# Performance work log

Hardware: AMD Instinct MI355X
Metric: run time of the kernel (lower is better)

Reference implementation:

```python
import jax, jax.numpy as jnp
import numpy as np
from jax import lax

BETA = 5.0
THRESHOLD = 20.0

def softplus5(x):
    # torch nn.Softplus(beta=5, threshold=20)
    return jnp.where(BETA * x > THRESHOLD, x, jax.nn.softplus(BETA * x) / BETA)

def setup_inputs() -> dict:
    key = jax.random.key(0)
    k1, k2, k3, k4, k5 = jax.random.split(key, 5)
    B, T, I, H = 128, 256, 1024, 1024
    stdv = 1.0 / np.sqrt(H)
    x = jax.random.normal(k1, (B, T, I), dtype=jnp.float32)
    hidden = jnp.zeros((2, B, H), dtype=jnp.float32)
    Wi = jax.random.uniform(k2, (H, I), dtype=jnp.float32, minval=-stdv, maxval=stdv)
    bi = jax.random.uniform(k3, (H,), dtype=jnp.float32, minval=-stdv, maxval=stdv)
    Wh = jax.random.uniform(k4, (H, H), dtype=jnp.float32, minval=-stdv, maxval=stdv)
    bh = jax.random.uniform(k5, (H,), dtype=jnp.float32, minval=-stdv, maxval=stdv)
    return {"x": x, "hidden": hidden, "Wi": Wi, "bi": bi, "Wh": Wh, "bh": bh}

def reference(x, hidden, Wi, bi, Wh, bh):
    # x: [B, T, I] (batch_first) -> time-major [T, B, I]
    xt = jnp.swapaxes(x, 0, 1)
    T = xt.shape[0]
    # precompute i2h for all steps (one big GEMM)
    pre = jnp.einsum('tbi,hi->tbh', xt, Wi) + bi  # [T, B, H]

    def step(h, p):
        h_next = softplus5(p + h @ Wh.T + bh)
        return h_next, h_next

    _, fwd = lax.scan(step, hidden[0], pre)          # fwd[t]: hidden after step t
    _, bwd = lax.scan(step, hidden[1], pre[::-1])    # bwd[j]: backward hidden at time i = T-1-j
    # bi_outputs appended for i = T-1 ... 0: position t holds cat(outputs[(T-1-t)-16], bwd[t])
    idx = (jnp.arange(T)[::-1] - 16) % T  # Python negative-index wrap of outputs[i-16]
    out = jnp.concatenate([fwd[idx], bwd], axis=-1)  # [T, B, 2H]
    return jnp.swapaxes(out, 0, 1)                   # [B, T, 2H]
```

## Files before the change

### kernel.cpp

```cpp
#include <hip/hip_runtime.h>
#include <stddef.h>

using short8 = __attribute__((ext_vector_type(8))) short;
using f32x4  = __attribute__((ext_vector_type(4))) float;
using f32x16 = __attribute__((ext_vector_type(16))) float;
using u16x4  = __attribute__((ext_vector_type(4))) unsigned short;

__device__ __forceinline__ unsigned short cvt_bf16(float f) {
    unsigned u = __builtin_bit_cast(unsigned, f);
    u += 0x7fffu + ((u >> 16) & 1u);
    return (unsigned short)(u >> 16);
}

__device__ __forceinline__ void gload_lds16(const void* g, void* l) {
    __builtin_amdgcn_global_load_lds(
        (const __attribute__((address_space(1))) unsigned*)g,
        (__attribute__((address_space(3))) unsigned*)l, 16, 0, 0);
}

#define MFMA16(a, b, c) __builtin_amdgcn_mfma_f32_16x16x32_bf16((a), (b), (c), 0, 0, 0)
#define MFMA32(a, b, c) __builtin_amdgcn_mfma_f32_32x32x16_bf16((a), (b), (c), 0, 0, 0)

__global__ __launch_bounds__(256) void convert_w(const float* __restrict__ Wi,
                                                 const float* __restrict__ Wh,
                                                 unsigned short* __restrict__ Wib,
                                                 unsigned short* __restrict__ Whb) {
    const float* src = blockIdx.y ? Wh : Wi;
    unsigned short* dst = blockIdx.y ? Whb : Wib;
    int base = blockIdx.x * 2048 + threadIdx.x * 8;
#pragma unroll
    for (int c = 0; c < 2; ++c) {
        float4 v = *(const float4*)(src + base + c * 4);
        u16x4 o;
        o.x = cvt_bf16(v.x); o.y = cvt_bf16(v.y); o.z = cvt_bf16(v.z); o.w = cvt_bf16(v.w);
        *(u16x4*)(dst + base + c * 4) = o;
    }
}

__global__ __launch_bounds__(256) void init_h(const float* __restrict__ hidden,
                                              unsigned short* __restrict__ h0,
                                              unsigned* __restrict__ flags) {
    int row = blockIdx.x;
    int tid = threadIdx.x;
    float4 v = *(const float4*)(hidden + (size_t)row * 1024 + tid * 4);
    u16x4 o;
    o.x = cvt_bf16(v.x); o.y = cvt_bf16(v.y); o.z = cvt_bf16(v.z); o.w = cvt_bf16(v.w);
    *(u16x4*)(h0 + (size_t)row * 1024 + tid * 4) = o;
    if (blockIdx.x == 0 && tid < 256) flags[tid] = 0;
}

__global__ __launch_bounds__(256) void pre_gemm(const float* __restrict__ x,
                                                const unsigned short* __restrict__ Wib,
                                                const float* __restrict__ bi,
                                                float* __restrict__ pre) {
    __shared__ unsigned short Alds[128 * 64];
    __shared__ unsigned short Blds[128 * 64];
    const int tid  = threadIdx.x;
    const int lane = tid & 63, wid = tid >> 6;
    const int wr = wid >> 1, wc = wid & 1;
    const int t  = blockIdx.y;
    const int n0 = blockIdx.x * 128;

    f32x4 acc[4][4] = {};

    for (int kt = 0; kt < 16; ++kt) {
        const int k0 = kt * 64;
        __syncthreads();
#pragma unroll
        for (int c = 0; c < 8; ++c) {
            int flat = c * 256 + tid;
            int row = flat >> 4;
            int seg = flat & 15;
            float4 v = *(const float4*)(x + (size_t)row * 262144 + (size_t)t * 1024 + k0 + seg * 4);
            u16x4 h;
            h.x = cvt_bf16(v.x); h.y = cvt_bf16(v.y); h.z = cvt_bf16(v.z); h.w = cvt_bf16(v.w);
            *(u16x4*)&Alds[row * 64 + seg * 4] = h;
        }
#pragma unroll
        for (int c = 0; c < 4; ++c) {
            int flat = c * 256 + tid;
            int row = flat >> 3;
            int seg = flat & 7;
            gload_lds16(Wib + (size_t)(n0 + row) * 1024 + k0 + seg * 8, &Blds[flat * 8]);
        }
        __syncthreads();
#pragma unroll
        for (int ks = 0; ks < 2; ++ks) {
            short8 a[4], b[4];
#pragma unroll
            for (int i = 0; i < 4; ++i)
                a[i] = *(const short8*)&Alds[(wr * 64 + i * 16 + (lane & 15)) * 64 + ks * 32 + (lane >> 4) * 8];
#pragma unroll
            for (int j = 0; j < 4; ++j)
                b[j] = *(const short8*)&Blds[(wc * 64 + j * 16 + (lane & 15)) * 64 + ks * 32 + (lane >> 4) * 8];
#pragma unroll
            for (int i = 0; i < 4; ++i)
#pragma unroll
                for (int j = 0; j < 4; ++j)
                    acc[i][j] = MFMA16(a[i], b[j], acc[i][j]);
        }
    }
    const int rbase = wr * 64 + (lane >> 4) * 4;
    const int cbase = n0 + wc * 64 + (lane & 15);
#pragma unroll
    for (int i = 0; i < 4; ++i) {
#pragma unroll
        for (int j = 0; j < 4; ++j) {
            int n = cbase + j * 16;
            float bv = bi[n];
#pragma unroll
            for (int r = 0; r < 4; ++r) {
                int m = rbase + i * 16 + r;
                pre[((size_t)t * 128 + m) * 1024 + n] = acc[i][j][r] + bv;
            }
        }
    }
}

__global__ __launch_bounds__(256, 1) void rnn_scan(const unsigned short* __restrict__ Whb,
                                                   const float* __restrict__ pre,
                                                   const float* __restrict__ bh,
                                                   unsigned short* __restrict__ ha,
                                                   unsigned short* __restrict__ hb,
                                                   float* __restrict__ out,
                                                   unsigned* __restrict__ flags) {
    __shared__ unsigned short Alds[32 * 1024];
    __shared__ float Red[4][1024];

    const int tid  = threadIdx.x;
    const int lane = tid & 63, wid = tid >> 6;
    const int bid  = blockIdx.x;
    const int g    = bid & 7, ni = bid >> 3;
    const int m0   = g * 32, n0 = ni * 32;
    const bool fwd = (g < 4);
    unsigned* gflags = flags + g * 32;

    short8 bfrag[16];
    {
        const unsigned short* bp = Whb + (size_t)(n0 + (lane & 31)) * 1024
                                 + wid * 256 + (lane >> 5) * 8;
#pragma unroll
        for (int ks = 0; ks < 16; ++ks)
            bfrag[ks] = *(const short8*)(bp + ks * 16);
    }

    const int mloc = tid >> 3;
    const int nloc = (tid & 7) * 4;
    const int m    = m0 + mloc;
    const int b    = m & 127;
    const int n    = n0 + nloc;
    const float4 bh4 = *(const float4*)(bh + n);
    float* outp      = out + (size_t)b * 524288 + (fwd ? 0 : 1024) + n;
    const float* prebase = pre + (size_t)b * 1024 + n;

    const char* aswz_base = (const char*)Alds + (lane & 31) * 2048;
    const int   aswz      = (lane & 7) << 4;
    const int   kb0       = wid * 512 + (lane >> 5) * 16;

    for (int s = 0; s < 256; ++s) {
        const unsigned short* hin = (s & 1) ? hb : ha;
        unsigned short* hout      = (s & 1) ? ha : hb;
        const int prow = fwd ? s : 255 - s;
        float4 pv = *(const float4*)(prebase + (size_t)prow * 131072);

        if (s > 0) {
            if (tid < 64) {
                int fuel = 1 << 20;
                unsigned v;
                do {
                    v = __hip_atomic_load(&gflags[lane & 31], __ATOMIC_RELAXED,
                                          __HIP_MEMORY_SCOPE_AGENT);
                } while (!__all((int)(v >= (unsigned)s)) && --fuel);
            }
            __syncthreads();
        }

        {
            const unsigned long long* hsrc =
                (const unsigned long long*)(hin + (size_t)m0 * 1024);
            const int colswz = tid * 8;
            unsigned long long tmp[32];
#pragma unroll
            for (int i = 0; i < 32; ++i)
                tmp[i] = __hip_atomic_load(&hsrc[(size_t)i * 256 + tid],
                                           __ATOMIC_RELAXED, __HIP_MEMORY_SCOPE_AGENT);
#pragma unroll
            for (int i = 0; i < 32; ++i)
                *(unsigned long long*)((char*)Alds + i * 2048
                                       + (colswz ^ ((i & 7) << 4))) = tmp[i];
        }
        __syncthreads();

        f32x16 acc0 = {}, acc1 = {};
#pragma unroll
        for (int ks = 0; ks < 16; ++ks) {
            short8 a = *(const short8*)(aswz_base + ((kb0 + ks * 32) ^ aswz));
            if (ks & 1) acc1 = MFMA32(a, bfrag[ks], acc1);
            else        acc0 = MFMA32(a, bfrag[ks], acc0);
        }
        f32x16 acc = acc0 + acc1;
#pragma unroll
        for (int r = 0; r < 16; ++r) {
            int row = (r & 3) + 8 * (r >> 2) + 4 * (lane >> 5);
            Red[wid][row * 32 + (lane & 31)] = acc[r];
        }
        __syncthreads();

        f32x4 ov;
        {
            const int o = tid * 4;
            float4 q0 = *(const float4*)&Red[0][o];
            float4 q1 = *(const float4*)&Red[1][o];
            float4 q2 = *(const float4*)&Red[2][o];
            float4 q3 = *(const float4*)&Red[3][o];
            float vv[4] = { q0.x + q1.x + q2.x + q3.x + pv.x + bh4.x,
                            q0.y + q1.y + q2.y + q3.y + pv.y + bh4.y,
                            q0.z + q1.z + q2.z + q3.z + pv.z + bh4.z,
                            q0.w + q1.w + q2.w + q3.w + pv.w + bh4.w };
            u16x4 hh;
#pragma unroll
            for (int j = 0; j < 4; ++j) {
                float xv = vv[j];
                float hv = (5.0f * xv > 20.0f) ? xv : 0.2f * log1pf(__expf(5.0f * xv));
                ov[j] = hv;
                hh[j] = cvt_bf16(hv);
            }
            __hip_atomic_store((unsigned long long*)(hout + (size_t)m * 1024 + n),
                               __builtin_bit_cast(unsigned long long, hh),
                               __ATOMIC_RELAXED, __HIP_MEMORY_SCOPE_AGENT);
        }
        asm volatile("s_waitcnt vmcnt(0)" ::: "memory");
        __syncthreads();

        if (s < 255 && tid == 0)
            __hip_atomic_store(&gflags[ni], (unsigned)(s + 1),
                               __ATOMIC_RELAXED, __HIP_MEMORY_SCOPE_AGENT);

        int tout = fwd ? ((239 - s) & 255) : s;
        __builtin_nontemporal_store(ov, (f32x4*)(outp + (size_t)tout * 2048));
    }
}

extern "C" void kernel_launch(void* const* d_in, const int* in_sizes, int n_in,
                              void* d_out, int out_size, void* d_ws, size_t ws_size,
                              hipStream_t stream) {
    const float* x      = (const float*)d_in[0];
    const float* hidden = (const float*)d_in[1];
    const float* Wi     = (const float*)d_in[2];
    const float* bi     = (const float*)d_in[3];
    const float* Wh     = (const float*)d_in[4];
    const float* bh     = (const float*)d_in[5];
    float* out = (float*)d_out;

    char* ws = (char*)d_ws;
    float*          pre = (float*)ws;
    unsigned short* Wib = (unsigned short*)(ws + 134217728);
    unsigned short* Whb = (unsigned short*)(ws + 136314880);
    unsigned short* ha  = (unsigned short*)(ws + 138412032);
    unsigned short* hb  = (unsigned short*)(ws + 138936320);
    unsigned*     flags = (unsigned*)(ws + 139460608);

    convert_w<<<dim3(512, 2), 256, 0, stream>>>(Wi, Wh, Wib, Whb);
    init_h<<<256, 256, 0, stream>>>(hidden, ha, flags);
    pre_gemm<<<dim3(8, 256), 256, 0, stream>>>(x, Wib, bi, pre);
    rnn_scan<<<256, 256, 0, stream>>>(Whb, pre, bh, ha, hb, out, flags);
}
```

Baseline: 1.214 ms.

## Use XCD-local cache-scoped sync when all group blocks share one XCD

At startup each block records its XCD id, read from a hardware register, into a workspace slot. Each 32-block group then checks whether all its members landed on the same XCD. If they did, the per-step flag polling and hidden-state exchange use plain loads and stores with the sc0 bit instead of agent-scope atomics, so traffic can stay in the shared L2 rather than going through device-coherent paths. The output stores also change from nontemporal to regular stores. The risks are relying on block placement, adding a startup handshake, and coherence correctness if the co-location check is wrong.

```diff
diff --git a/kernel.cpp b/kernel.cpp
--- a/kernel.cpp
+++ b/kernel.cpp
@@ -46,7 +46,9 @@
     u16x4 o;
     o.x = cvt_bf16(v.x); o.y = cvt_bf16(v.y); o.z = cvt_bf16(v.z); o.w = cvt_bf16(v.w);
     *(u16x4*)(h0 + (size_t)row * 1024 + tid * 4) = o;
-    if (blockIdx.x == 0 && tid < 256) flags[tid] = 0;
+    if (blockIdx.x == 0) {
+        for (int i = tid; i < 512; i += 256) flags[i] = 0;
+    }
 }
 
 __global__ __launch_bounds__(256) void pre_gemm(const float* __restrict__ x,
@@ -126,6 +128,7 @@
                                                    unsigned* __restrict__ flags) {
     __shared__ unsigned short Alds[32 * 1024];
     __shared__ float Red[4][1024];
+    __shared__ int coloc_sh;
 
     const int tid  = threadIdx.x;
     const int lane = tid & 63, wid = tid >> 6;
@@ -133,7 +136,25 @@
     const int g    = bid & 7, ni = bid >> 3;
     const int m0   = g * 32, n0 = ni * 32;
     const bool fwd = (g < 4);
-    unsigned* gflags = flags + g * 32;
+    unsigned* gflags  = flags + g * 32;
+    unsigned* xcdslot = flags + 256;
+
+    if (tid == 0) {
+        unsigned x = __builtin_amdgcn_s_getreg(6164);
+        __hip_atomic_store(&xcdslot[bid], x + 1u, __ATOMIC_RELAXED, __HIP_MEMORY_SCOPE_AGENT);
+    }
+    if (tid < 64) {
+        unsigned v; int fuel = 1 << 22;
+        do {
+            v = __hip_atomic_load(&xcdslot[g * 32 + (lane & 31)],
+                                  __ATOMIC_RELAXED, __HIP_MEMORY_SCOPE_AGENT);
+        } while (__any((int)(v == 0u)) && --fuel);
+        unsigned v0 = __shfl(v, 0);
+        int c = __all((int)(v == v0));
+        if (tid == 0) coloc_sh = c;
+    }
+    __syncthreads();
+    const int coloc = coloc_sh;
 
     short8 bfrag[16];
     {
@@ -165,12 +186,19 @@
 
         if (s > 0) {
             if (tid < 64) {
-                int fuel = 1 << 20;
+                const unsigned* fp = &gflags[lane & 31];
+                int fuel = 1 << 22;
                 unsigned v;
-                do {
-                    v = __hip_atomic_load(&gflags[lane & 31], __ATOMIC_RELAXED,
-                                          __HIP_MEMORY_SCOPE_AGENT);
-                } while (!__all((int)(v >= (unsigned)s)) && --fuel);
+                if (coloc) {
+                    do {
+                        asm volatile("global_load_dword %0, %1, off sc0\n\ts_waitcnt vmcnt(0)"
+                                     : "=v"(v) : "v"(fp) : "memory");
+                    } while (!__all((int)(v >= (unsigned)s)) && --fuel);
+                } else {
+                    do {
+                        v = __hip_atomic_load(fp, __ATOMIC_RELAXED, __HIP_MEMORY_SCOPE_AGENT);
+                    } while (!__all((int)(v >= (unsigned)s)) && --fuel);
+                }
             }
             __syncthreads();
         }
@@ -178,12 +206,21 @@
         {
             const unsigned long long* hsrc =
                 (const unsigned long long*)(hin + (size_t)m0 * 1024);
+            unsigned long long tmp[32];
+            if (coloc) {
+#pragma unroll
+                for (int i = 0; i < 32; ++i)
+                    asm volatile("global_load_dwordx2 %0, %1, off sc0"
+                                 : "=v"(tmp[i]) : "v"(hsrc + (size_t)i * 256 + tid) : "memory");
+                asm volatile("s_waitcnt vmcnt(0)" ::: "memory");
+                __builtin_amdgcn_sched_barrier(0);
+            } else {
+#pragma unroll
+                for (int i = 0; i < 32; ++i)
+                    tmp[i] = __hip_atomic_load(&hsrc[(size_t)i * 256 + tid],
+                                               __ATOMIC_RELAXED, __HIP_MEMORY_SCOPE_AGENT);
+            }
             const int colswz = tid * 8;
-            unsigned long long tmp[32];
-#pragma unroll
-            for (int i = 0; i < 32; ++i)
-                tmp[i] = __hip_atomic_load(&hsrc[(size_t)i * 256 + tid],
-                                           __ATOMIC_RELAXED, __HIP_MEMORY_SCOPE_AGENT);
 #pragma unroll
             for (int i = 0; i < 32; ++i)
                 *(unsigned long long*)((char*)Alds + i * 2048
@@ -225,19 +262,31 @@
                 ov[j] = hv;
                 hh[j] = cvt_bf16(hv);
             }
-            __hip_atomic_store((unsigned long long*)(hout + (size_t)m * 1024 + n),
-                               __builtin_bit_cast(unsigned long long, hh),
-                               __ATOMIC_RELAXED, __HIP_MEMORY_SCOPE_AGENT);
+            unsigned long long hv64 = __builtin_bit_cast(unsigned long long, hh);
+            unsigned short* hp = hout + (size_t)m * 1024 + n;
+            if (coloc) {
+                asm volatile("global_store_dwordx2 %0, %1, off"
+                             :: "v"(hp), "v"(hv64) : "memory");
+            } else {
+                __hip_atomic_store((unsigned long long*)hp, hv64,
+                                   __ATOMIC_RELAXED, __HIP_MEMORY_SCOPE_AGENT);
+            }
         }
         asm volatile("s_waitcnt vmcnt(0)" ::: "memory");
         __syncthreads();
 
-        if (s < 255 && tid == 0)
-            __hip_atomic_store(&gflags[ni], (unsigned)(s + 1),
-                               __ATOMIC_RELAXED, __HIP_MEMORY_SCOPE_AGENT);
+        if (s < 255 && tid == 0) {
+            if (coloc) {
+                asm volatile("global_store_dword %0, %1, off"
+                             :: "v"(&gflags[ni]), "v"((unsigned)(s + 1)) : "memory");
+            } else {
+                __hip_atomic_store(&gflags[ni], (unsigned)(s + 1),
+                                   __ATOMIC_RELAXED, __HIP_MEMORY_SCOPE_AGENT);
+            }
+        }
 
         int tout = fwd ? ((239 - s) & 255) : s;
-        __builtin_nontemporal_store(ov, (f32x4*)(outp + (size_t)tout * 2048));
+        *(f32x4*)(outp + (size_t)tout * 2048) = ov;
     }
 }
 
```

New measurement: 1.239 ms. +2.1%, slower.

## Restructure RNN scan to full-K per wave, fewer blocks and flags

Applied to the files above, without the earlier changes.

The recurrent scan changes from 256 blocks, each splitting K across four waves and reducing through LDS, to 64 blocks where each wave owns 32 output columns over the full K=1024. Each wave keeps 64 weight fragments in registers. This removes the cross-wave LDS reduction and one barrier per step, and cuts the number of flags each group polls from 32 to 8, which should lower per-step synchronisation latency. The costs are much higher register pressure (64 short8 fragments), 4x more MFMAs in sequence per wave, and fewer CUs sharing the work. Output stores also change from nontemporal to plain stores.

```diff
diff --git a/kernel.cpp b/kernel.cpp
--- a/kernel.cpp
+++ b/kernel.cpp
@@ -46,7 +46,9 @@
     u16x4 o;
     o.x = cvt_bf16(v.x); o.y = cvt_bf16(v.y); o.z = cvt_bf16(v.z); o.w = cvt_bf16(v.w);
     *(u16x4*)(h0 + (size_t)row * 1024 + tid * 4) = o;
-    if (blockIdx.x == 0 && tid < 256) flags[tid] = 0;
+    if (blockIdx.x == 0) {
+        for (int i = tid; i < 512; i += 256) flags[i] = 0;
+    }
 }
 
 __global__ __launch_bounds__(256) void pre_gemm(const float* __restrict__ x,
@@ -125,107 +127,95 @@
                                                    float* __restrict__ out,
                                                    unsigned* __restrict__ flags) {
     __shared__ unsigned short Alds[32 * 1024];
-    __shared__ float Red[4][1024];
 
     const int tid  = threadIdx.x;
     const int lane = tid & 63, wid = tid >> 6;
     const int bid  = blockIdx.x;
-    const int g    = bid & 7, ni = bid >> 3;
-    const int m0   = g * 32, n0 = ni * 32;
+    const int g    = bid & 7, ci = bid >> 3;
+    const int m0   = g * 32;
+    const int nw   = ci * 128 + wid * 32;
     const bool fwd = (g < 4);
-    unsigned* gflags = flags + g * 32;
-
-    short8 bfrag[16];
+    unsigned* gflags = flags + g * 8;
+
+    short8 wfrag[64];
     {
-        const unsigned short* bp = Whb + (size_t)(n0 + (lane & 31)) * 1024
-                                 + wid * 256 + (lane >> 5) * 8;
-#pragma unroll
-        for (int ks = 0; ks < 16; ++ks)
-            bfrag[ks] = *(const short8*)(bp + ks * 16);
-    }
-
-    const int mloc = tid >> 3;
-    const int nloc = (tid & 7) * 4;
-    const int m    = m0 + mloc;
-    const int b    = m & 127;
-    const int n    = n0 + nloc;
-    const float4 bh4 = *(const float4*)(bh + n);
-    float* outp      = out + (size_t)b * 524288 + (fwd ? 0 : 1024) + n;
-    const float* prebase = pre + (size_t)b * 1024 + n;
-
-    const char* aswz_base = (const char*)Alds + (lane & 31) * 2048;
-    const int   aswz      = (lane & 7) << 4;
-    const int   kb0       = wid * 512 + (lane >> 5) * 16;
+        const unsigned short* bp = Whb + (size_t)(nw + (lane & 31)) * 1024 + (lane >> 5) * 8;
+#pragma unroll
+        for (int ks = 0; ks < 64; ++ks)
+            wfrag[ks] = *(const short8*)(bp + ks * 16);
+    }
+
+    const int m   = lane & 31;
+    const int mg  = m0 + m;
+    const int b   = mg & 127;
+    const int nhi = (lane >> 5) * 4;
+    f32x4 bh4[4];
+#pragma unroll
+    for (int q = 0; q < 4; ++q)
+        bh4[q] = *(const f32x4*)(bh + nw + nhi + q * 8);
+    const float* prebase = pre + (size_t)b * 1024 + nw + nhi;
+    float* outbase       = out + (size_t)b * 524288 + (fwd ? 0 : 1024) + nw + nhi;
+
+    const char* arow = (const char*)Alds + m * 2048;
+    const int   swz  = (m & 15) << 4;
 
     for (int s = 0; s < 256; ++s) {
         const unsigned short* hin = (s & 1) ? hb : ha;
         unsigned short* hout      = (s & 1) ? ha : hb;
         const int prow = fwd ? s : 255 - s;
-        float4 pv = *(const float4*)(prebase + (size_t)prow * 131072);
+
+        f32x4 pv[4];
+#pragma unroll
+        for (int q = 0; q < 4; ++q)
+            pv[q] = *(const f32x4*)(prebase + (size_t)prow * 131072 + q * 8);
 
         if (s > 0) {
-            if (tid < 64) {
-                int fuel = 1 << 20;
-                unsigned v;
-                do {
-                    v = __hip_atomic_load(&gflags[lane & 31], __ATOMIC_RELAXED,
-                                          __HIP_MEMORY_SCOPE_AGENT);
-                } while (!__all((int)(v >= (unsigned)s)) && --fuel);
-            }
-            __syncthreads();
+            int fuel = 1 << 22;
+            unsigned v;
+            do {
+                v = __hip_atomic_load(&gflags[lane & 7], __ATOMIC_RELAXED,
+                                      __HIP_MEMORY_SCOPE_AGENT);
+            } while (!__all((int)(v >= (unsigned)s)) && --fuel);
         }
 
         {
             const unsigned long long* hsrc =
                 (const unsigned long long*)(hin + (size_t)m0 * 1024);
-            const int colswz = tid * 8;
             unsigned long long tmp[32];
 #pragma unroll
             for (int i = 0; i < 32; ++i)
                 tmp[i] = __hip_atomic_load(&hsrc[(size_t)i * 256 + tid],
                                            __ATOMIC_RELAXED, __HIP_MEMORY_SCOPE_AGENT);
+            const int colswz = tid * 8;
 #pragma unroll
             for (int i = 0; i < 32; ++i)
                 *(unsigned long long*)((char*)Alds + i * 2048
-                                       + (colswz ^ ((i & 7) << 4))) = tmp[i];
+                                       + (colswz ^ ((i & 15) << 4))) = tmp[i];
         }
         __syncthreads();
 
         f32x16 acc0 = {}, acc1 = {};
-#pragma unroll
-        for (int ks = 0; ks < 16; ++ks) {
-            short8 a = *(const short8*)(aswz_base + ((kb0 + ks * 32) ^ aswz));
-            if (ks & 1) acc1 = MFMA32(a, bfrag[ks], acc1);
-            else        acc0 = MFMA32(a, bfrag[ks], acc0);
+        const int khi = (lane >> 5) * 16;
+#pragma unroll
+        for (int ks = 0; ks < 64; ++ks) {
+            short8 hf = *(const short8*)(arow + ((ks * 32 + khi) ^ swz));
+            if (ks & 1) acc1 = MFMA32(wfrag[ks], hf, acc1);
+            else        acc0 = MFMA32(wfrag[ks], hf, acc0);
         }
         f32x16 acc = acc0 + acc1;
-#pragma unroll
-        for (int r = 0; r < 16; ++r) {
-            int row = (r & 3) + 8 * (r >> 2) + 4 * (lane >> 5);
-            Red[wid][row * 32 + (lane & 31)] = acc[r];
-        }
-        __syncthreads();
-
-        f32x4 ov;
-        {
-            const int o = tid * 4;
-            float4 q0 = *(const float4*)&Red[0][o];
-            float4 q1 = *(const float4*)&Red[1][o];
-            float4 q2 = *(const float4*)&Red[2][o];
-            float4 q3 = *(const float4*)&Red[3][o];
-            float vv[4] = { q0.x + q1.x + q2.x + q3.x + pv.x + bh4.x,
-                            q0.y + q1.y + q2.y + q3.y + pv.y + bh4.y,
-                            q0.z + q1.z + q2.z + q3.z + pv.z + bh4.z,
-                            q0.w + q1.w + q2.w + q3.w + pv.w + bh4.w };
+
+        f32x4 ov[4];
+#pragma unroll
+        for (int q = 0; q < 4; ++q) {
             u16x4 hh;
 #pragma unroll
             for (int j = 0; j < 4; ++j) {
-                float xv = vv[j];
+                float xv = acc[q * 4 + j] + pv[q][j] + bh4[q][j];
                 float hv = (5.0f * xv > 20.0f) ? xv : 0.2f * log1pf(__expf(5.0f * xv));
-                ov[j] = hv;
+                ov[q][j] = hv;
                 hh[j] = cvt_bf16(hv);
             }
-            __hip_atomic_store((unsigned long long*)(hout + (size_t)m * 1024 + n),
+            __hip_atomic_store((unsigned long long*)(hout + (size_t)mg * 1024 + nw + nhi + q * 8),
                                __builtin_bit_cast(unsigned long long, hh),
                                __ATOMIC_RELAXED, __HIP_MEMORY_SCOPE_AGENT);
         }
@@ -233,11 +223,13 @@
         __syncthreads();
 
         if (s < 255 && tid == 0)
-            __hip_atomic_store(&gflags[ni], (unsigned)(s + 1),
+            __hip_atomic_store(&gflags[ci], (unsigned)(s + 1),
                                __ATOMIC_RELAXED, __HIP_MEMORY_SCOPE_AGENT);
 
-        int tout = fwd ? ((239 - s) & 255) : s;
-        __builtin_nontemporal_store(ov, (f32x4*)(outp + (size_t)tout * 2048));
+        const int tout = fwd ? ((239 - s) & 255) : s;
+#pragma unroll
+        for (int q = 0; q < 4; ++q)
+            *(f32x4*)(outbase + (size_t)tout * 2048 + q * 8) = ov[q];
     }
 }
 
@@ -263,5 +255,5 @@
     convert_w<<<dim3(512, 2), 256, 0, stream>>>(Wi, Wh, Wib, Whb);
     init_h<<<256, 256, 0, stream>>>(hidden, ha, flags);
     pre_gemm<<<dim3(8, 256), 256, 0, stream>>>(x, Wib, bi, pre);
-    rnn_scan<<<256, 256, 0, stream>>>(Whb, pre, bh, ha, hb, out, flags);
-}
+    rnn_scan<<<64, 256, 0, stream>>>(Whb, pre, bh, ha, hb, out, flags);
+}
```

Result: slower. 2.695 ms (+122.0%).

## Load recurrent A fragments directly from global and finalize in one wave

Applied to the files above, without the earlier changes.

Drops the LDS staging of the hidden-state tile, so each wave spins on the flags itself and loads its MFMA A-operand fragments straight from global memory with atomic loads. The epilogue (reduction, softplus, h store, flag publish, output store) now runs only in wave 0, which removes two block-wide barriers per step. The trade-off is uncoalesced 8-byte global loads and four separate spinning waves, a single wave doing all the epilogue work, and a larger spin limit. It also looks like a hazard on the Red buffer, since the next step's writes are no longer fenced against wave 0's reads.

```diff
diff --git a/kernel.cpp b/kernel.cpp
--- a/kernel.cpp
+++ b/kernel.cpp
@@ -5,6 +5,8 @@
 using f32x4  = __attribute__((ext_vector_type(4))) float;
 using f32x16 = __attribute__((ext_vector_type(16))) float;
 using u16x4  = __attribute__((ext_vector_type(4))) unsigned short;
+
+struct U128 { unsigned long long a, b; };
 
 __device__ __forceinline__ unsigned short cvt_bf16(float f) {
     unsigned u = __builtin_bit_cast(unsigned, f);
@@ -46,7 +48,9 @@
     u16x4 o;
     o.x = cvt_bf16(v.x); o.y = cvt_bf16(v.y); o.z = cvt_bf16(v.z); o.w = cvt_bf16(v.w);
     *(u16x4*)(h0 + (size_t)row * 1024 + tid * 4) = o;
-    if (blockIdx.x == 0 && tid < 256) flags[tid] = 0;
+    if (blockIdx.x == 0) {
+        for (int i = tid; i < 512; i += 256) flags[i] = 0;
+    }
 }
 
 __global__ __launch_bounds__(256) void pre_gemm(const float* __restrict__ x,
@@ -124,7 +128,6 @@
                                                    unsigned short* __restrict__ hb,
                                                    float* __restrict__ out,
                                                    unsigned* __restrict__ flags) {
-    __shared__ unsigned short Alds[32 * 1024];
     __shared__ float Red[4][1024];
 
     const int tid  = threadIdx.x;
@@ -144,57 +147,55 @@
             bfrag[ks] = *(const short8*)(bp + ks * 16);
     }
 
-    const int mloc = tid >> 3;
-    const int nloc = (tid & 7) * 4;
-    const int m    = m0 + mloc;
-    const int b    = m & 127;
-    const int n    = n0 + nloc;
-    const float4 bh4 = *(const float4*)(bh + n);
-    float* outp      = out + (size_t)b * 524288 + (fwd ? 0 : 1024) + n;
-    const float* prebase = pre + (size_t)b * 1024 + n;
-
-    const char* aswz_base = (const char*)Alds + (lane & 31) * 2048;
-    const int   aswz      = (lane & 7) << 4;
-    const int   kb0       = wid * 512 + (lane >> 5) * 16;
+    const size_t arow_off = (size_t)(lane & 31) * 2048 + wid * 512 + (lane >> 5) * 16;
+
+    const int em  = lane >> 1;
+    const int en  = (lane & 1) * 16;
+    const int emg = m0 + em;
+    const int eb  = emg & 127;
+    f32x4 bh4[4];
+#pragma unroll
+    for (int q = 0; q < 4; ++q)
+        bh4[q] = *(const f32x4*)(bh + n0 + en + q * 4);
+    const float* prebase = pre + (size_t)eb * 1024 + n0 + en;
+    float* outbase       = out + (size_t)eb * 524288 + (fwd ? 0 : 1024) + n0 + en;
 
     for (int s = 0; s < 256; ++s) {
         const unsigned short* hin = (s & 1) ? hb : ha;
         unsigned short* hout      = (s & 1) ? ha : hb;
         const int prow = fwd ? s : 255 - s;
-        float4 pv = *(const float4*)(prebase + (size_t)prow * 131072);
+
+        f32x4 pv[4];
+        if (wid == 0) {
+#pragma unroll
+            for (int q = 0; q < 4; ++q)
+                pv[q] = *(const f32x4*)(prebase + (size_t)prow * 131072 + q * 4);
+        }
 
         if (s > 0) {
-            if (tid < 64) {
-                int fuel = 1 << 20;
-                unsigned v;
-                do {
-                    v = __hip_atomic_load(&gflags[lane & 31], __ATOMIC_RELAXED,
-                                          __HIP_MEMORY_SCOPE_AGENT);
-                } while (!__all((int)(v >= (unsigned)s)) && --fuel);
-            }
-            __syncthreads();
-        }
-
-        {
-            const unsigned long long* hsrc =
-                (const unsigned long long*)(hin + (size_t)m0 * 1024);
-            const int colswz = tid * 8;
-            unsigned long long tmp[32];
-#pragma unroll
-            for (int i = 0; i < 32; ++i)
-                tmp[i] = __hip_atomic_load(&hsrc[(size_t)i * 256 + tid],
-                                           __ATOMIC_RELAXED, __HIP_MEMORY_SCOPE_AGENT);
-#pragma unroll
-            for (int i = 0; i < 32; ++i)
-                *(unsigned long long*)((char*)Alds + i * 2048
-                                       + (colswz ^ ((i & 7) << 4))) = tmp[i];
-        }
-        __syncthreads();
+            int fuel = 1 << 22;
+            unsigned v;
+            do {
+                v = __hip_atomic_load(&gflags[lane & 31], __ATOMIC_RELAXED,
+                                      __HIP_MEMORY_SCOPE_AGENT);
+            } while (!__all((int)(v >= (unsigned)s)) && --fuel);
+        }
+
+        const char* hsrc = (const char*)(hin + (size_t)m0 * 1024) + arow_off;
+        unsigned long long alo[16], ahi[16];
+#pragma unroll
+        for (int i = 0; i < 16; ++i) {
+            alo[i] = __hip_atomic_load((const unsigned long long*)(hsrc + i * 32),
+                                       __ATOMIC_RELAXED, __HIP_MEMORY_SCOPE_AGENT);
+            ahi[i] = __hip_atomic_load((const unsigned long long*)(hsrc + i * 32 + 8),
+                                       __ATOMIC_RELAXED, __HIP_MEMORY_SCOPE_AGENT);
+        }
 
         f32x16 acc0 = {}, acc1 = {};
 #pragma unroll
         for (int ks = 0; ks < 16; ++ks) {
-            short8 a = *(const short8*)(aswz_base + ((kb0 + ks * 32) ^ aswz));
+            U128 t2{alo[ks], ahi[ks]};
+            short8 a = __builtin_bit_cast(short8, t2);
             if (ks & 1) acc1 = MFMA32(a, bfrag[ks], acc1);
             else        acc0 = MFMA32(a, bfrag[ks], acc0);
         }
@@ -206,38 +207,39 @@
         }
         __syncthreads();
 
-        f32x4 ov;
-        {
-            const int o = tid * 4;
-            float4 q0 = *(const float4*)&Red[0][o];
-            float4 q1 = *(const float4*)&Red[1][o];
-            float4 q2 = *(const float4*)&Red[2][o];
-            float4 q3 = *(const float4*)&Red[3][o];
-            float vv[4] = { q0.x + q1.x + q2.x + q3.x + pv.x + bh4.x,
-                            q0.y + q1.y + q2.y + q3.y + pv.y + bh4.y,
-                            q0.z + q1.z + q2.z + q3.z + pv.z + bh4.z,
-                            q0.w + q1.w + q2.w + q3.w + pv.w + bh4.w };
-            u16x4 hh;
-#pragma unroll
-            for (int j = 0; j < 4; ++j) {
-                float xv = vv[j];
-                float hv = (5.0f * xv > 20.0f) ? xv : 0.2f * log1pf(__expf(5.0f * xv));
-                ov[j] = hv;
-                hh[j] = cvt_bf16(hv);
+        if (wid == 0) {
+            f32x4 ov[4];
+#pragma unroll
+            for (int q = 0; q < 4; ++q) {
+                const int o = (em * 32 + en) + q * 4;
+                f32x4 v0 = *(const f32x4*)&Red[0][o];
+                f32x4 v1 = *(const f32x4*)&Red[1][o];
+                f32x4 v2 = *(const f32x4*)&Red[2][o];
+                f32x4 v3 = *(const f32x4*)&Red[3][o];
+                f32x4 vv = v0 + v1 + v2 + v3 + pv[q] + bh4[q];
+                u16x4 hh;
+#pragma unroll
+                for (int j = 0; j < 4; ++j) {
+                    float xv = vv[j];
+                    float hv = (5.0f * xv > 20.0f) ? xv : 0.2f * log1pf(__expf(5.0f * xv));
+                    ov[q][j] = hv;
+                    hh[j] = cvt_bf16(hv);
+                }
+                __hip_atomic_store(
+                    (unsigned long long*)(hout + (size_t)emg * 1024 + n0 + en + q * 4),
+                    __builtin_bit_cast(unsigned long long, hh),
+                    __ATOMIC_RELAXED, __HIP_MEMORY_SCOPE_AGENT);
             }
-            __hip_atomic_store((unsigned long long*)(hout + (size_t)m * 1024 + n),
-                               __builtin_bit_cast(unsigned long long, hh),
-                               __ATOMIC_RELAXED, __HIP_MEMORY_SCOPE_AGENT);
-        }
-        asm volatile("s_waitcnt vmcnt(0)" ::: "memory");
-        __syncthreads();
-
-        if (s < 255 && tid == 0)
-            __hip_atomic_store(&gflags[ni], (unsigned)(s + 1),
-                               __ATOMIC_RELAXED, __HIP_MEMORY_SCOPE_AGENT);
-
-        int tout = fwd ? ((239 - s) & 255) : s;
-        __builtin_nontemporal_store(ov, (f32x4*)(outp + (size_t)tout * 2048));
+            asm volatile("s_waitcnt vmcnt(0)" ::: "memory");
+            if (lane == 0 && s < 255)
+                __hip_atomic_store(&gflags[ni], (unsigned)(s + 1),
+                                   __ATOMIC_RELAXED, __HIP_MEMORY_SCOPE_AGENT);
+            const int tout = fwd ? ((239 - s) & 255) : s;
+#pragma unroll
+            for (int q = 0; q < 4; ++q)
+                __builtin_nontemporal_store(ov[q],
+                    (f32x4*)(outbase + (size_t)tout * 2048 + q * 4));
+        }
     }
 }
 
```

After: 2.825 ms. +132.7%, slower.
